# Optimization experiments

Hardware: AMD Instinct MI355X
Metric: run time of the kernel (lower is better)

Reference implementation:

```python
import jax, jax.numpy as jnp
import numpy as np

A = 1.0          # jacobi a
B = 1.0          # jacobi b
BASE_ALPHA = 2.0
K = 10           # polynomial order
N = 16384        # nodes
C = 32           # channels


def setup_inputs() -> dict:
    key = jax.random.key(0)
    k1, k2 = jax.random.split(key, 2)
    x = jax.random.normal(k1, (N, C), dtype=jnp.float32)
    # dense graph operator (stand-in for a normalized laplacian); scaled so spectrum is O(1)
    L = jax.random.normal(k2, (N, N), dtype=jnp.float32) / np.float32(np.sqrt(N))
    conv_params = jnp.full((K + 1,), min(1.0 / BASE_ALPHA, 1.0), dtype=jnp.float32)
    comb_params = jnp.ones((K + 1, C), dtype=jnp.float32)
    return {"x": x, "L": L, "conv_params": conv_params, "comb_params": comb_params}


def reference(x, L, conv_params, comb_params):
    a, b = A, B
    alpha = BASE_ALPHA * jnp.tanh(conv_params)  # [K+1] learned step sizes
    polys = [x]  # P_0 = x
    if K >= 1:
        # with l=-1, r=1: (r+l)/(r-l)=0, 1/(r-l)=0.5
        c1 = alpha[0] * (a - b) / 2.0
        c2 = alpha[0] * (a + b + 2.0) / 2.0
        polys.append(c1 * x + c2 * (L @ x))
    for i in range(2, K + 1):
        div = 2.0 * i * (i + a + b) * (2.0 * i + a + b - 2.0)
        r1 = (2.0 * i + a + b) * (2.0 * i + a + b - 1.0) * (2.0 * i + a + b - 2.0) / div
        r2 = (2.0 * i + a + b - 1.0) * (a * a - b * b) / div
        r3 = 2.0 * (i + a - 1.0) * (i + b - 1.0) * (2.0 * i + a + b) / div
        c1 = alpha[i - 1] * r1                      # multiplies L @ P_{i-1} (coef1, since 2/(r-l)=1)
        c2 = alpha[i - 1] * r2                      # coef2 (the (r+l)/(r-l) term vanishes)
        c3 = alpha[i - 1] * alpha[i - 2] * r3       # coef_3
        polys.append(c1 * (L @ polys[-1]) + c2 * polys[-1] - c3 * polys[-2])
    # y = sum_k comb[k] (broadcast over nodes) * P_k  -- avoids materializing the stacked [K+1,N,C]
    y = polys[0] * comb_params[0][None, :]
    for k in range(1, K + 1):
        y = y + comb_params[k][None, :] * polys[k]
    return y
```

## Files before the change

### kernel.cpp

```cpp
#include <hip/hip_runtime.h>
#include <math.h>


#define NN 16384
#define CC 32
#define KPOLY 10
#define NSPLIT 16
#define NTK (NN / 32)

typedef _Float16 half8 __attribute__((ext_vector_type(8)));
typedef float f32x4 __attribute__((ext_vector_type(4)));
typedef unsigned int u32x4 __attribute__((ext_vector_type(4)));
typedef unsigned int u32x2 __attribute__((ext_vector_type(2)));

union U16 {
  u32x4 u;
  half8 h;
};
union H4 {
  _Float16 h[4];
  u32x2 u;
};

__global__ __launch_bounds__(256) void conv_pack_gemm1(const float* __restrict__ L,
                                                       _Float16* __restrict__ Lf,
                                                       const _Float16* __restrict__ Ph,
                                                       float* __restrict__ part) {
  __shared__ __align__(16) _Float16 lds[16 * 1024];
  const int tid = threadIdx.x;
  const int tr = blockIdx.x >> 4;
  const int sc = blockIdx.x & 15;
  const float* src = L + (size_t)tr * 16 * NN + (size_t)sc * 1024;

#pragma unroll
  for (int j = 0; j < 16; ++j) {
    const int flat = j * 256 + tid;
    const int r = flat >> 8;
    const int cu = flat & 255;
    f32x4 v = __builtin_nontemporal_load(
        reinterpret_cast<const f32x4*>(src + (size_t)r * NN) + cu);
    H4 o;
    o.h[0] = (_Float16)v.x;
    o.h[1] = (_Float16)v.y;
    o.h[2] = (_Float16)v.z;
    o.h[3] = (_Float16)v.w;
    const int u = (cu >> 1) ^ (r & 7);
    *reinterpret_cast<u32x2*>(&lds[r * 1024 + u * 8 + (cu & 1) * 4]) = o.u;
  }
  __syncthreads();

  const int lane = tid & 63;
  const int wave = tid >> 6;
  const int r = lane & 15;
  const int lg = lane >> 4;

  f32x4 acc0 = (f32x4){0.f, 0.f, 0.f, 0.f};
  f32x4 acc1 = (f32x4){0.f, 0.f, 0.f, 0.f};
#pragma unroll
  for (int i = 0; i < 8; ++i) {
    const int tkl = wave * 8 + i;
    const int u = (tkl * 4 + lg) ^ (r & 7);
    U16 aval;
    aval.u = *reinterpret_cast<const u32x4*>(&lds[r * 1024 + u * 8]);
    const size_t tk = (size_t)sc * 32 + tkl;
    __builtin_nontemporal_store(
        aval.u, reinterpret_cast<u32x4*>(Lf + ((size_t)tr * NTK + tk) * 512) + lane);
    const int kb = sc * 128 + tkl * 4 + lg;
    U16 b0, b1;
    b0.u = *reinterpret_cast<const u32x4*>(Ph + (size_t)kb * 256 + (size_t)r * 8);
    b1.u = *reinterpret_cast<const u32x4*>(Ph + (size_t)kb * 256 + (size_t)(16 + r) * 8);
    acc0 = __builtin_amdgcn_mfma_f32_16x16x32_f16(aval.h, b0.h, acc0, 0, 0, 0);
    acc1 = __builtin_amdgcn_mfma_f32_16x16x32_f16(aval.h, b1.h, acc1, 0, 0, 0);
  }
  __syncthreads();

  float* red = reinterpret_cast<float*>(lds);
#pragma unroll
  for (int j = 0; j < 4; ++j) {
    red[wave * 512 + (lg * 4 + j) * 32 + r] = acc0[j];
    red[wave * 512 + (lg * 4 + j) * 32 + 16 + r] = acc1[j];
  }
  __syncthreads();

  const int e = tid * 2;
  float2 s0 = *reinterpret_cast<const float2*>(&red[e]);
  float2 s1 = *reinterpret_cast<const float2*>(&red[512 + e]);
  float2 s2 = *reinterpret_cast<const float2*>(&red[1024 + e]);
  float2 s3 = *reinterpret_cast<const float2*>(&red[1536 + e]);
  float2 s = make_float2(s0.x + s1.x + s2.x + s3.x, s0.y + s1.y + s2.y + s3.y);
  *reinterpret_cast<float2*>(part + (size_t)sc * NN * CC + (size_t)tr * 16 * CC + e) = s;
}

__global__ __launch_bounds__(256, 4) void gemm_poly(
    const _Float16* __restrict__ Lf, const _Float16* __restrict__ PhIn,
    const float* __restrict__ Pprev, const float* __restrict__ Pprev2,
    float* __restrict__ Pnew, _Float16* __restrict__ PhOut, float* __restrict__ y,
    const float* __restrict__ conv, const float* __restrict__ comb_row, float r1,
    float r2, float r3, int ia, int ib) {
  const int tid = threadIdx.x;
  const int lane = tid & 63;
  const int wave = tid >> 6;
  const int tr = blockIdx.x;
  const int l15 = lane & 15;
  const int lg = lane >> 4;

  const int tk0 = wave * 128;
  const u32x4* Ap =
      reinterpret_cast<const u32x4*>(Lf + ((size_t)tr * NTK + tk0) * 512) + lane;
  const _Float16* Bbase = PhIn + (size_t)(tk0 * 4 + lg) * 256 + (size_t)l15 * 8;

  f32x4 acc0 = (f32x4){0.f, 0.f, 0.f, 0.f};
  f32x4 acc1 = (f32x4){0.f, 0.f, 0.f, 0.f};

  U16 A0, A1, B00, B01, B10, B11;
  A0.u = __builtin_nontemporal_load(Ap);
  B00.u = *reinterpret_cast<const u32x4*>(Bbase);
  B01.u = *reinterpret_cast<const u32x4*>(Bbase + 128);

  for (int kk = 0; kk < 128; kk += 2) {
    A1.u = __builtin_nontemporal_load(Ap + (kk + 1) * 64);
    B10.u = *reinterpret_cast<const u32x4*>(Bbase + (size_t)(kk + 1) * 1024);
    B11.u = *reinterpret_cast<const u32x4*>(Bbase + (size_t)(kk + 1) * 1024 + 128);
    acc0 = __builtin_amdgcn_mfma_f32_16x16x32_f16(A0.h, B00.h, acc0, 0, 0, 0);
    acc1 = __builtin_amdgcn_mfma_f32_16x16x32_f16(A0.h, B01.h, acc1, 0, 0, 0);
    if (kk + 2 < 128) {
      A0.u = __builtin_nontemporal_load(Ap + (kk + 2) * 64);
      B00.u = *reinterpret_cast<const u32x4*>(Bbase + (size_t)(kk + 2) * 1024);
      B01.u = *reinterpret_cast<const u32x4*>(Bbase + (size_t)(kk + 2) * 1024 + 128);
    }
    acc0 = __builtin_amdgcn_mfma_f32_16x16x32_f16(A1.h, B10.h, acc0, 0, 0, 0);
    acc1 = __builtin_amdgcn_mfma_f32_16x16x32_f16(A1.h, B11.h, acc1, 0, 0, 0);
  }

  __shared__ float red[4 * 512];
#pragma unroll
  for (int j = 0; j < 4; ++j) {
    red[wave * 512 + (lg * 4 + j) * 32 + l15] = acc0[j];
    red[wave * 512 + (lg * 4 + j) * 32 + 16 + l15] = acc1[j];
  }
  __syncthreads();

  const int e = tid * 2;
  float2 s0 = *reinterpret_cast<const float2*>(&red[e]);
  float2 s1 = *reinterpret_cast<const float2*>(&red[512 + e]);
  float2 s2 = *reinterpret_cast<const float2*>(&red[1024 + e]);
  float2 s3 = *reinterpret_cast<const float2*>(&red[1536 + e]);
  float2 t = make_float2(s0.x + s1.x + s2.x + s3.x, s0.y + s1.y + s2.y + s3.y);

  const int row = e >> 5;
  const int c = e & 31;
  const int n = tr * 16 + row;
  const size_t g = (size_t)n * CC + c;

  const float a1 = 2.f * tanhf(conv[ia]);
  const float a2 = 2.f * tanhf(conv[ib]);
  const float cL = a1 * r1;
  const float cP = a1 * r2;
  const float cPP = a1 * a2 * r3;

  float2 pp = *reinterpret_cast<const float2*>(Pprev + g);
  float2 p2 = *reinterpret_cast<const float2*>(Pprev2 + g);
  float2 pn;
  pn.x = cL * t.x + cP * pp.x - cPP * p2.x;
  pn.y = cL * t.y + cP * pp.y - cPP * p2.y;
  *reinterpret_cast<float2*>(Pnew + g) = pn;

  const size_t pb = (size_t)(n >> 3) * 256 + (size_t)c * 8 + (n & 7);
  PhOut[pb] = (_Float16)pn.x;
  PhOut[pb + 8] = (_Float16)pn.y;

  float2 cb = *reinterpret_cast<const float2*>(comb_row + c);
  float2 yv = *reinterpret_cast<float2*>(y + g);
  yv.x = fmaf(cb.x, pn.x, yv.x);
  yv.y = fmaf(cb.y, pn.y, yv.y);
  *reinterpret_cast<float2*>(y + g) = yv;
}

__global__ __launch_bounds__(256) void init_kernel(const float* __restrict__ x,
                                                   const float* __restrict__ comb,
                                                   float* __restrict__ y,
                                                   _Float16* __restrict__ Ph) {
  int idx = blockIdx.x * blockDim.x + threadIdx.x;
  float4 xv = reinterpret_cast<const float4*>(x)[idx];
  int c4 = (idx & 7) << 2;
  int n = idx >> 3;
  float4 cb = *reinterpret_cast<const float4*>(comb + c4);
  reinterpret_cast<float4*>(y)[idx] =
      make_float4(xv.x * cb.x, xv.y * cb.y, xv.z * cb.z, xv.w * cb.w);
  size_t pb = (size_t)(n >> 3) * 256 + (size_t)c4 * 8 + (n & 7);
  Ph[pb] = (_Float16)xv.x;
  Ph[pb + 8] = (_Float16)xv.y;
  Ph[pb + 16] = (_Float16)xv.z;
  Ph[pb + 24] = (_Float16)xv.w;
}

__global__ __launch_bounds__(256) void poly_update(
    const float* __restrict__ part, float* __restrict__ Pnew,
    const float* __restrict__ Pprev, float* __restrict__ y,
    _Float16* __restrict__ PhOut, const float* __restrict__ conv,
    const float* __restrict__ comb_row, float r1, float r2, int ia) {
  int idx = blockIdx.x * blockDim.x + threadIdx.x;
  float a1 = 2.f * tanhf(conv[ia]);
  float cL = a1 * r1;
  float cP = a1 * r2;

  float4 t = make_float4(0.f, 0.f, 0.f, 0.f);
#pragma unroll
  for (int s = 0; s < NSPLIT; ++s) {
    float4 p = reinterpret_cast<const float4*>(part)[(size_t)s * (NN * CC / 4) + idx];
    t.x += p.x;
    t.y += p.y;
    t.z += p.z;
    t.w += p.w;
  }

  float4 pp = reinterpret_cast<const float4*>(Pprev)[idx];
  float4 pn;
  pn.x = cL * t.x + cP * pp.x;
  pn.y = cL * t.y + cP * pp.y;
  pn.z = cL * t.z + cP * pp.z;
  pn.w = cL * t.w + cP * pp.w;
  reinterpret_cast<float4*>(Pnew)[idx] = pn;

  int c4 = (idx & 7) << 2;
  int n = idx >> 3;
  size_t pb = (size_t)(n >> 3) * 256 + (size_t)c4 * 8 + (n & 7);
  PhOut[pb] = (_Float16)pn.x;
  PhOut[pb + 8] = (_Float16)pn.y;
  PhOut[pb + 16] = (_Float16)pn.z;
  PhOut[pb + 24] = (_Float16)pn.w;

  float4 cb = *reinterpret_cast<const float4*>(comb_row + c4);
  float4 yv = reinterpret_cast<float4*>(y)[idx];
  yv.x = fmaf(cb.x, pn.x, yv.x);
  yv.y = fmaf(cb.y, pn.y, yv.y);
  yv.z = fmaf(cb.z, pn.z, yv.z);
  yv.w = fmaf(cb.w, pn.w, yv.w);
  reinterpret_cast<float4*>(y)[idx] = yv;
}

static void jacobi_r(int i, double a, double b, float& r1, float& r2, float& r3) {
  double div = 2.0 * i * (i + a + b) * (2.0 * i + a + b - 2.0);
  r1 = (float)((2.0 * i + a + b) * (2.0 * i + a + b - 1.0) * (2.0 * i + a + b - 2.0) / div);
  r2 = (float)((2.0 * i + a + b - 1.0) * (a * a - b * b) / div);
  r3 = (float)(2.0 * (i + a - 1.0) * (i + b - 1.0) * (2.0 * i + a + b) / div);
}

extern "C" void kernel_launch(void* const* d_in, const int* in_sizes, int n_in,
                              void* d_out, int out_size, void* d_ws, size_t ws_size,
                              hipStream_t stream) {
  const float* x = (const float*)d_in[0];
  const float* Lm = (const float*)d_in[1];
  const float* conv = (const float*)d_in[2];
  const float* comb = (const float*)d_in[3];
  float* y = (float*)d_out;
  char* ws = (char*)d_ws;

  _Float16* Lf = (_Float16*)ws;
  float* part = (float*)(ws + 536870912ull);
  _Float16* PhA = (_Float16*)(ws + 536870912ull + 33554432ull);
  _Float16* PhB = PhA + (size_t)NN * CC;
  float* Pb0 = (float*)(ws + 536870912ull + 33554432ull + 4194304ull);
  float* Pb1 = Pb0 + (size_t)NN * CC;
  float* Pb2 = Pb1 + (size_t)NN * CC;
  float* bufs[3] = {Pb0, Pb1, Pb2};

  const double Aj = 1.0, Bj = 1.0;
  const int ew_blocks = NN * CC / 4 / 256;

  init_kernel<<<ew_blocks, 256, 0, stream>>>(x, comb, y, PhA);
  conv_pack_gemm1<<<16384, 256, 0, stream>>>(Lm, Lf, PhA, part);

  {
    float r1 = (float)((Aj + Bj + 2.0) / 2.0);
    float r2 = (float)((Aj - Bj) / 2.0);
    poly_update<<<ew_blocks, 256, 0, stream>>>(part, bufs[0], x, y, PhB, conv,
                                               comb + CC, r1, r2, 0);
  }

  const float* Pprev = bufs[0];
  const float* Pprev2 = x;
  for (int i = 2; i <= KPOLY; ++i) {
    float r1, r2, r3;
    jacobi_r(i, Aj, Bj, r1, r2, r3);
    float* Pn = bufs[(i - 1) % 3];
    const _Float16* PhIn = (i & 1) ? PhA : PhB;
    _Float16* PhOut = (i & 1) ? PhB : PhA;
    gemm_poly<<<NN / 16, 256, 0, stream>>>(Lf, PhIn, Pprev, Pprev2, Pn, PhOut, y,
                                           conv, comb + (size_t)i * CC, r1, r2, r3,
                                           i - 1, i - 2);
    Pprev2 = Pprev;
    Pprev = Pn;
  }
}
```

Baseline: 1.397 ms.

## Tile gemm_poly to 64 rows per block with 8 K-split waves

Each gemm_poly block now computes 64 output rows (four 16-row tiles) with 512 threads in 8 waves, each wave covering 64 K-tiles. Every B fragment loaded from the fp16 polynomial is reused across four A row tiles, so B traffic falls and more loads are in flight per wave. The reduction across waves uses a larger LDS buffer, and the epilogue works on float4. In exchange the kernel uses more registers and LDS, occupancy drops to one block per CU, and there are fewer blocks (256).

```diff
diff --git a/kernel.cpp b/kernel.cpp
--- a/kernel.cpp
+++ b/kernel.cpp
@@ -7,6 +7,7 @@
 #define KPOLY 10
 #define NSPLIT 16
 #define NTK (NN / 32)
+#define WTILES 64
 
 typedef _Float16 half8 __attribute__((ext_vector_type(8)));
 typedef float f32x4 __attribute__((ext_vector_type(4)));
@@ -91,7 +92,7 @@
   *reinterpret_cast<float2*>(part + (size_t)sc * NN * CC + (size_t)tr * 16 * CC + e) = s;
 }
 
-__global__ __launch_bounds__(256, 4) void gemm_poly(
+__global__ __launch_bounds__(512, 1) void gemm_poly(
     const _Float16* __restrict__ Lf, const _Float16* __restrict__ PhIn,
     const float* __restrict__ Pprev, const float* __restrict__ Pprev2,
     float* __restrict__ Pnew, _Float16* __restrict__ PhOut, float* __restrict__ y,
@@ -100,56 +101,77 @@
   const int tid = threadIdx.x;
   const int lane = tid & 63;
   const int wave = tid >> 6;
-  const int tr = blockIdx.x;
+  const int trb = blockIdx.x * 4;
   const int l15 = lane & 15;
   const int lg = lane >> 4;
-
-  const int tk0 = wave * 128;
-  const u32x4* Ap =
-      reinterpret_cast<const u32x4*>(Lf + ((size_t)tr * NTK + tk0) * 512) + lane;
+  const int tk0 = wave * WTILES;
+
+  const u32x4* Ap[4];
+#pragma unroll
+  for (int rt = 0; rt < 4; ++rt)
+    Ap[rt] = reinterpret_cast<const u32x4*>(
+                 Lf + ((size_t)(trb + rt) * NTK + tk0) * 512) +
+             lane;
   const _Float16* Bbase = PhIn + (size_t)(tk0 * 4 + lg) * 256 + (size_t)l15 * 8;
 
-  f32x4 acc0 = (f32x4){0.f, 0.f, 0.f, 0.f};
-  f32x4 acc1 = (f32x4){0.f, 0.f, 0.f, 0.f};
-
-  U16 A0, A1, B00, B01, B10, B11;
-  A0.u = __builtin_nontemporal_load(Ap);
-  B00.u = *reinterpret_cast<const u32x4*>(Bbase);
-  B01.u = *reinterpret_cast<const u32x4*>(Bbase + 128);
-
-  for (int kk = 0; kk < 128; kk += 2) {
-    A1.u = __builtin_nontemporal_load(Ap + (kk + 1) * 64);
-    B10.u = *reinterpret_cast<const u32x4*>(Bbase + (size_t)(kk + 1) * 1024);
-    B11.u = *reinterpret_cast<const u32x4*>(Bbase + (size_t)(kk + 1) * 1024 + 128);
-    acc0 = __builtin_amdgcn_mfma_f32_16x16x32_f16(A0.h, B00.h, acc0, 0, 0, 0);
-    acc1 = __builtin_amdgcn_mfma_f32_16x16x32_f16(A0.h, B01.h, acc1, 0, 0, 0);
-    if (kk + 2 < 128) {
-      A0.u = __builtin_nontemporal_load(Ap + (kk + 2) * 64);
-      B00.u = *reinterpret_cast<const u32x4*>(Bbase + (size_t)(kk + 2) * 1024);
-      B01.u = *reinterpret_cast<const u32x4*>(Bbase + (size_t)(kk + 2) * 1024 + 128);
+  f32x4 acc[4][2];
+#pragma unroll
+  for (int rt = 0; rt < 4; ++rt)
+#pragma unroll
+    for (int ct = 0; ct < 2; ++ct) acc[rt][ct] = (f32x4){0.f, 0.f, 0.f, 0.f};
+
+  U16 A[2][4], B[2][2];
+#pragma unroll
+  for (int rt = 0; rt < 4; ++rt) A[0][rt].u = __builtin_nontemporal_load(Ap[rt]);
+#pragma unroll
+  for (int ct = 0; ct < 2; ++ct)
+    B[0][ct].u = *reinterpret_cast<const u32x4*>(Bbase + ct * 128);
+
+#pragma unroll
+  for (int kk = 0; kk < WTILES; ++kk) {
+    const int cur = kk & 1;
+    const int nxt = cur ^ 1;
+    if (kk < WTILES - 1) {
+#pragma unroll
+      for (int rt = 0; rt < 4; ++rt)
+        A[nxt][rt].u = __builtin_nontemporal_load(Ap[rt] + (kk + 1) * 64);
+#pragma unroll
+      for (int ct = 0; ct < 2; ++ct)
+        B[nxt][ct].u = *reinterpret_cast<const u32x4*>(
+            Bbase + (size_t)(kk + 1) * 1024 + ct * 128);
     }
-    acc0 = __builtin_amdgcn_mfma_f32_16x16x32_f16(A1.h, B10.h, acc0, 0, 0, 0);
-    acc1 = __builtin_amdgcn_mfma_f32_16x16x32_f16(A1.h, B11.h, acc1, 0, 0, 0);
-  }
-
-  __shared__ float red[4 * 512];
-#pragma unroll
-  for (int j = 0; j < 4; ++j) {
-    red[wave * 512 + (lg * 4 + j) * 32 + l15] = acc0[j];
-    red[wave * 512 + (lg * 4 + j) * 32 + 16 + l15] = acc1[j];
-  }
+#pragma unroll
+    for (int rt = 0; rt < 4; ++rt)
+#pragma unroll
+      for (int ct = 0; ct < 2; ++ct)
+        acc[rt][ct] = __builtin_amdgcn_mfma_f32_16x16x32_f16(A[cur][rt].h, B[cur][ct].h,
+                                                             acc[rt][ct], 0, 0, 0);
+  }
+
+  __shared__ float red[8][2048];
+#pragma unroll
+  for (int rt = 0; rt < 4; ++rt)
+#pragma unroll
+    for (int ct = 0; ct < 2; ++ct)
+#pragma unroll
+      for (int j = 0; j < 4; ++j)
+        red[wave][(rt * 16 + lg * 4 + j) * 32 + ct * 16 + l15] = acc[rt][ct][j];
   __syncthreads();
 
-  const int e = tid * 2;
-  float2 s0 = *reinterpret_cast<const float2*>(&red[e]);
-  float2 s1 = *reinterpret_cast<const float2*>(&red[512 + e]);
-  float2 s2 = *reinterpret_cast<const float2*>(&red[1024 + e]);
-  float2 s3 = *reinterpret_cast<const float2*>(&red[1536 + e]);
-  float2 t = make_float2(s0.x + s1.x + s2.x + s3.x, s0.y + s1.y + s2.y + s3.y);
-
-  const int row = e >> 5;
-  const int c = e & 31;
-  const int n = tr * 16 + row;
+  const int e0 = tid * 4;
+  float4 t = make_float4(0.f, 0.f, 0.f, 0.f);
+#pragma unroll
+  for (int w = 0; w < 8; ++w) {
+    float4 p = *reinterpret_cast<const float4*>(&red[w][e0]);
+    t.x += p.x;
+    t.y += p.y;
+    t.z += p.z;
+    t.w += p.w;
+  }
+
+  const int row = e0 >> 5;
+  const int c = e0 & 31;
+  const int n = blockIdx.x * 64 + row;
   const size_t g = (size_t)n * CC + c;
 
   const float a1 = 2.f * tanhf(conv[ia]);
@@ -158,22 +180,28 @@
   const float cP = a1 * r2;
   const float cPP = a1 * a2 * r3;
 
-  float2 pp = *reinterpret_cast<const float2*>(Pprev + g);
-  float2 p2 = *reinterpret_cast<const float2*>(Pprev2 + g);
-  float2 pn;
+  float4 pp = *reinterpret_cast<const float4*>(Pprev + g);
+  float4 p2 = *reinterpret_cast<const float4*>(Pprev2 + g);
+  float4 pn;
   pn.x = cL * t.x + cP * pp.x - cPP * p2.x;
   pn.y = cL * t.y + cP * pp.y - cPP * p2.y;
-  *reinterpret_cast<float2*>(Pnew + g) = pn;
+  pn.z = cL * t.z + cP * pp.z - cPP * p2.z;
+  pn.w = cL * t.w + cP * pp.w - cPP * p2.w;
+  *reinterpret_cast<float4*>(Pnew + g) = pn;
 
   const size_t pb = (size_t)(n >> 3) * 256 + (size_t)c * 8 + (n & 7);
   PhOut[pb] = (_Float16)pn.x;
   PhOut[pb + 8] = (_Float16)pn.y;
-
-  float2 cb = *reinterpret_cast<const float2*>(comb_row + c);
-  float2 yv = *reinterpret_cast<float2*>(y + g);
+  PhOut[pb + 16] = (_Float16)pn.z;
+  PhOut[pb + 24] = (_Float16)pn.w;
+
+  float4 cb = *reinterpret_cast<const float4*>(comb_row + c);
+  float4 yv = *reinterpret_cast<float4*>(y + g);
   yv.x = fmaf(cb.x, pn.x, yv.x);
   yv.y = fmaf(cb.y, pn.y, yv.y);
-  *reinterpret_cast<float2*>(y + g) = yv;
+  yv.z = fmaf(cb.z, pn.z, yv.z);
+  yv.w = fmaf(cb.w, pn.w, yv.w);
+  *reinterpret_cast<float4*>(y + g) = yv;
 }
 
 __global__ __launch_bounds__(256) void init_kernel(const float* __restrict__ x,
@@ -286,7 +314,7 @@
     float* Pn = bufs[(i - 1) % 3];
     const _Float16* PhIn = (i & 1) ? PhA : PhB;
     _Float16* PhOut = (i & 1) ? PhB : PhA;
-    gemm_poly<<<NN / 16, 256, 0, stream>>>(Lf, PhIn, Pprev, Pprev2, Pn, PhOut, y,
+    gemm_poly<<<NN / 64, 512, 0, stream>>>(Lf, PhIn, Pprev, Pprev2, Pn, PhOut, y,
                                            conv, comb + (size_t)i * CC, r1, r2, r3,
                                            i - 1, i - 2);
     Pprev2 = Pprev;
```

Result: faster. 1.127 ms (median of 2 runs) (-19.3%).
